# Performance work log

Hardware: AMD Instinct MI355X
Metric: run time of the kernel (lower is better)

Reference implementation:

```python
import jax, jax.numpy as jnp
import numpy as np

B, S, IN_F, OUT_F = 4, 2048, 4096, 4096
ALPHA = 0.01

def setup_inputs() -> dict:
    key = jax.random.key(0)
    k1, k2 = jax.random.split(key, 2)
    # int8-valued activations and weights (stored as int32 per harness dtype)
    x = jax.random.randint(k1, (B, S, IN_F), -127, 127, dtype=jnp.int32)
    weight = jax.random.randint(k2, (IN_F, OUT_F), -127, 127, dtype=jnp.int32)
    bias = jnp.zeros((1, OUT_F), dtype=jnp.float16)
    alpha = jnp.full((1,), ALPHA, dtype=jnp.float32)
    return {"x": x, "weight": weight, "bias": bias, "alpha": alpha}

def reference(x, weight, bias, alpha):
    # Faithful to forward's default (non-hybrid) path:
    # y = F.linear(x.float(), weight.t().float(), bias.float()) * alpha
    # F.linear(x, W^T) == x @ W, with W shape (in_features, out_features).
    x_shape = x.shape
    xf = x.reshape(-1, x_shape[-1]).astype(jnp.float32)          # [B*S, in]
    wf = weight.astype(jnp.float32)                               # [in, out]
    y = (xf @ wf + bias.astype(jnp.float32)) * alpha              # [B*S, out]
    return y.reshape(*x_shape[:-1], -1)                           # [B, S, out]
```

## Files before the change

kernel.cpp:

```cpp
#include <hip/hip_runtime.h>
#include <hip/hip_fp16.h>

using i32x4  = __attribute__((ext_vector_type(4)))  int;
using i32x16 = __attribute__((ext_vector_type(16))) int;

static constexpr int M  = 4 * 2048;
static constexpr int N  = 4096;
static constexpr int K  = 4096;
static constexpr int BM = 128, BN = 128, BK = 64;
static constexpr int NT = K / BK;
static constexpr int TILE = BM * BK;


__device__ __forceinline__ unsigned pack4(i32x4 v) {
  return (unsigned)((v.x & 255) | ((v.y & 255) << 8) | ((v.z & 255) << 16) | (v.w << 24));
}

__global__ __launch_bounds__(256) void pack_x_kernel(const int* __restrict__ x,
                                                     unsigned char* __restrict__ wa) {
  unsigned g = blockIdx.x * 256 + threadIdx.x;
  unsigned tile = g >> 9, gt = g & 511;
  unsigned kg = gt >> 7, row = gt & 127;
  unsigned br = tile >> 6, kt = tile & 63;
  const int* src = x + ((size_t)(br * 128 + row) * K + kt * 64 + kg * 16);
  i32x4 v0 = *(const i32x4*)(src + 0);
  i32x4 v1 = *(const i32x4*)(src + 4);
  i32x4 v2 = *(const i32x4*)(src + 8);
  i32x4 v3 = *(const i32x4*)(src + 12);
  i32x4 d;
  d.x = (int)pack4(v0); d.y = (int)pack4(v1); d.z = (int)pack4(v2); d.w = (int)pack4(v3);
  *(i32x4*)(wa + (size_t)g * 16) = d;
}

__global__ __launch_bounds__(256) void pack_w_kernel(const int* __restrict__ w,
                                                     unsigned char* __restrict__ wb) {
  unsigned g = blockIdx.x * 256 + threadIdx.x;
  unsigned tile = g >> 9, gt = g & 511;
  unsigned kg = gt >> 7, col = gt & 127;
  unsigned bn = tile >> 6, kt = tile & 63;
  unsigned n  = bn * 128 + col;
  unsigned k0 = kt * 64 + kg * 16;
  const int* src = w + (size_t)k0 * N + n;
  i32x4 d;
#pragma unroll
  for (int j = 0; j < 4; ++j) {
    int b0 = src[(size_t)(j * 4 + 0) * N];
    int b1 = src[(size_t)(j * 4 + 1) * N];
    int b2 = src[(size_t)(j * 4 + 2) * N];
    int b3 = src[(size_t)(j * 4 + 3) * N];
    d[j] = (b0 & 255) | ((b1 & 255) << 8) | ((b2 & 255) << 16) | (b3 << 24);
  }
  *(i32x4*)(wb + (size_t)g * 16) = d;
}


__device__ __forceinline__ void gload_lds16(const void* g, void* l) {
  __builtin_amdgcn_global_load_lds((const __attribute__((address_space(1))) unsigned int*)g,
                                   (__attribute__((address_space(3))) unsigned int*)l,
                                   16, 0, 0);
}

__global__ __launch_bounds__(256) void gemm_i8(const unsigned char* __restrict__ wa,
                                               const unsigned char* __restrict__ wb,
                                               const __half* __restrict__ bias,
                                               const float* __restrict__ alphaP,
                                               float* __restrict__ out) {
  __shared__ __align__(16) unsigned char As[2][TILE];
  __shared__ __align__(16) unsigned char Bs[2][TILE];

  const int tid  = threadIdx.x;
  const int lane = tid & 63;
  const int w    = tid >> 6;
  const int wr   = w >> 1, wc = w & 1;
  const int bc   = blockIdx.x, br = blockIdx.y;

  const unsigned char* ga = wa + (size_t)br * NT * TILE;
  const unsigned char* gb = wb + (size_t)bc * NT * TILE;

  i32x16 acc[2][2] = {};

  const int l31 = lane & 31;
  const int kgl = lane >> 5;

  auto stage = [&](int buf, int t) {
    const unsigned char* at = ga + (size_t)t * TILE;
    const unsigned char* bt = gb + (size_t)t * TILE;
#pragma unroll
    for (int i = 0; i < 2; ++i) {
      const int seg = w * 2 + i;
      gload_lds16(at + seg * 1024 + lane * 16, &As[buf][seg * 1024]);
      gload_lds16(bt + seg * 1024 + lane * 16, &Bs[buf][seg * 1024]);
    }
  };

  stage(0, 0);
  asm volatile("s_waitcnt vmcnt(0)" ::: "memory");
  __syncthreads();

  int cur = 0;
  for (int t = 0; t < NT; ++t) {
    if (t + 1 < NT) stage(cur ^ 1, t + 1);
#pragma unroll
    for (int c = 0; c < 2; ++c) {
      const int kg = c * 2 + kgl;
      const unsigned char* Ap = &As[cur][kg * 2048];
      const unsigned char* Bp = &Bs[cur][kg * 2048];
      i32x4 a0 = *(const i32x4*)(Ap + (wr * 64 + l31) * 16);
      i32x4 a1 = *(const i32x4*)(Ap + (wr * 64 + 32 + l31) * 16);
      i32x4 b0 = *(const i32x4*)(Bp + (wc * 64 + l31) * 16);
      i32x4 b1 = *(const i32x4*)(Bp + (wc * 64 + 32 + l31) * 16);
      acc[0][0] = __builtin_amdgcn_mfma_i32_32x32x32_i8(a0, b0, acc[0][0], 0, 0, 0);
      acc[0][1] = __builtin_amdgcn_mfma_i32_32x32x32_i8(a0, b1, acc[0][1], 0, 0, 0);
      acc[1][0] = __builtin_amdgcn_mfma_i32_32x32x32_i8(a1, b0, acc[1][0], 0, 0, 0);
      acc[1][1] = __builtin_amdgcn_mfma_i32_32x32x32_i8(a1, b1, acc[1][1], 0, 0, 0);
    }
    asm volatile("s_waitcnt vmcnt(0)" ::: "memory");
    __syncthreads();
    cur ^= 1;
  }

  const float alpha = *alphaP;
  const int row0 = br * 128 + wr * 64 + 4 * kgl;
  const int col0 = bc * 128 + wc * 64 + l31;
#pragma unroll
  for (int ni = 0; ni < 2; ++ni) {
    const int col = col0 + ni * 32;
    const float bf = __half2float(bias[col]);
#pragma unroll
    for (int mi = 0; mi < 2; ++mi) {
#pragma unroll
      for (int r = 0; r < 16; ++r) {
        const int row = row0 + mi * 32 + (r & 3) + 8 * (r >> 2);
        out[(size_t)row * N + col] = ((float)acc[mi][ni][r] + bf) * alpha;
      }
    }
  }
}

extern "C" void kernel_launch(void* const* d_in, const int* in_sizes, int n_in,
                              void* d_out, int out_size, void* d_ws, size_t ws_size,
                              hipStream_t stream) {
  const int*    x     = (const int*)d_in[0];
  const int*    wgt   = (const int*)d_in[1];
  const __half* bias  = (const __half*)d_in[2];
  const float*  alpha = (const float*)d_in[3];
  float*        out   = (float*)d_out;

  unsigned char* wa = (unsigned char*)d_ws;
  unsigned char* wb = wa + (size_t)M * K;

  pack_x_kernel<<<(M * (size_t)K / 16) / 256, 256, 0, stream>>>(x, wa);
  pack_w_kernel<<<(N * (size_t)K / 16) / 256, 256, 0, stream>>>(wgt, wb);

  dim3 grid(N / BN, M / BM);
  gemm_i8<<<grid, 256, 0, stream>>>(wa, wb, bias, alpha, out);
}
```

Measured before the change: 232.8 us.

## Enlarge GEMM tiles to 256x256 with 3-stage LDS pipeline and block swizzle

Doubles the block tile to 256x256 with 512 threads (8 waves, each 128x64), raising arithmetic intensity per LDS/global byte. Replaces the double buffer with a three-buffer prefetch pipeline using partial vmcnt waits, preloads fragments to registers before issuing the next stage, and raises MFMA priority. Adds a grid swizzle for L2 locality and repacks the pack kernels to the new tile layout. Risks higher register pressure (128 accumulator VGPRs per lane) and 96KB LDS limiting occupancy.

```diff
diff --git a/kernel.cpp b/kernel.cpp
--- a/kernel.cpp
+++ b/kernel.cpp
@@ -7,7 +7,7 @@
 static constexpr int M  = 4 * 2048;
 static constexpr int N  = 4096;
 static constexpr int K  = 4096;
-static constexpr int BM = 128, BN = 128, BK = 64;
+static constexpr int BM = 256, BN = 256, BK = 64;
 static constexpr int NT = K / BK;
 static constexpr int TILE = BM * BK;
 
@@ -19,10 +19,11 @@
 __global__ __launch_bounds__(256) void pack_x_kernel(const int* __restrict__ x,
                                                      unsigned char* __restrict__ wa) {
   unsigned g = blockIdx.x * 256 + threadIdx.x;
-  unsigned tile = g >> 9, gt = g & 511;
-  unsigned kg = gt >> 7, row = gt & 127;
-  unsigned br = tile >> 6, kt = tile & 63;
-  const int* src = x + ((size_t)(br * 128 + row) * K + kt * 64 + kg * 16);
+  unsigned row = g & 255;
+  unsigned kg  = (g >> 8) & 3;
+  unsigned kt  = (g >> 10) & 63;
+  unsigned br  = g >> 16;
+  const int* src = x + ((size_t)(br * 256 + row) * K + kt * 64 + kg * 16);
   i32x4 v0 = *(const i32x4*)(src + 0);
   i32x4 v1 = *(const i32x4*)(src + 4);
   i32x4 v2 = *(const i32x4*)(src + 8);
@@ -35,11 +36,12 @@
 __global__ __launch_bounds__(256) void pack_w_kernel(const int* __restrict__ w,
                                                      unsigned char* __restrict__ wb) {
   unsigned g = blockIdx.x * 256 + threadIdx.x;
-  unsigned tile = g >> 9, gt = g & 511;
-  unsigned kg = gt >> 7, col = gt & 127;
-  unsigned bn = tile >> 6, kt = tile & 63;
-  unsigned n  = bn * 128 + col;
-  unsigned k0 = kt * 64 + kg * 16;
+  unsigned col = g & 255;
+  unsigned kg  = (g >> 8) & 3;
+  unsigned kt  = (g >> 10) & 63;
+  unsigned bn  = g >> 16;
+  unsigned n   = bn * 256 + col;
+  unsigned k0  = kt * 64 + kg * 16;
   const int* src = w + (size_t)k0 * N + n;
   i32x4 d;
 #pragma unroll
@@ -60,74 +62,94 @@
                                    16, 0, 0);
 }
 
-__global__ __launch_bounds__(256) void gemm_i8(const unsigned char* __restrict__ wa,
-                                               const unsigned char* __restrict__ wb,
-                                               const __half* __restrict__ bias,
-                                               const float* __restrict__ alphaP,
-                                               float* __restrict__ out) {
-  __shared__ __align__(16) unsigned char As[2][TILE];
-  __shared__ __align__(16) unsigned char Bs[2][TILE];
+#define FENCE()   asm volatile("" ::: "memory")
+#define BARRIER() do { FENCE(); __builtin_amdgcn_s_barrier(); FENCE(); } while (0)
+
+__global__ __launch_bounds__(512, 2) void gemm_i8(const unsigned char* __restrict__ wa,
+                                                  const unsigned char* __restrict__ wb,
+                                                  const __half* __restrict__ bias,
+                                                  const float* __restrict__ alphaP,
+                                                  float* __restrict__ out) {
+  __shared__ __align__(16) unsigned char As[3][TILE];
+  __shared__ __align__(16) unsigned char Bs[3][TILE];
 
   const int tid  = threadIdx.x;
   const int lane = tid & 63;
   const int w    = tid >> 6;
-  const int wr   = w >> 1, wc = w & 1;
-  const int bc   = blockIdx.x, br = blockIdx.y;
+  const int wr   = w >> 2, wc = w & 3;
+  const int l31  = lane & 31;
+  const int kgl  = lane >> 5;
+
+  const int bid = blockIdx.x;
+  const int swz = (bid & 7) * 64 + (bid >> 3);
+  const int bc  = swz & 15;
+  const int br  = swz >> 4;
 
   const unsigned char* ga = wa + (size_t)br * NT * TILE;
   const unsigned char* gb = wb + (size_t)bc * NT * TILE;
 
-  i32x16 acc[2][2] = {};
-
-  const int l31 = lane & 31;
-  const int kgl = lane >> 5;
-
   auto stage = [&](int buf, int t) {
     const unsigned char* at = ga + (size_t)t * TILE;
     const unsigned char* bt = gb + (size_t)t * TILE;
-#pragma unroll
-    for (int i = 0; i < 2; ++i) {
-      const int seg = w * 2 + i;
-      gload_lds16(at + seg * 1024 + lane * 16, &As[buf][seg * 1024]);
-      gload_lds16(bt + seg * 1024 + lane * 16, &Bs[buf][seg * 1024]);
-    }
+    gload_lds16(at + w * 1024 + lane * 16,        &As[buf][w * 1024]);
+    gload_lds16(at + 8192 + w * 1024 + lane * 16, &As[buf][8192 + w * 1024]);
+    gload_lds16(bt + w * 1024 + lane * 16,        &Bs[buf][w * 1024]);
+    gload_lds16(bt + 8192 + w * 1024 + lane * 16, &Bs[buf][8192 + w * 1024]);
   };
 
   stage(0, 0);
-  asm volatile("s_waitcnt vmcnt(0)" ::: "memory");
-  __syncthreads();
+  stage(1, 1);
+  stage(2, 2);
 
-  int cur = 0;
+  i32x16 acc[4][2] = {};
+
+  int buf = 0;
   for (int t = 0; t < NT; ++t) {
-    if (t + 1 < NT) stage(cur ^ 1, t + 1);
+    if (t + 2 < NT)      asm volatile("s_waitcnt vmcnt(8)" ::: "memory");
+    else if (t + 1 < NT) asm volatile("s_waitcnt vmcnt(4)" ::: "memory");
+    else                 asm volatile("s_waitcnt vmcnt(0)" ::: "memory");
+    BARRIER();
+
+    i32x4 a[2][4], b[2][2];
 #pragma unroll
-    for (int c = 0; c < 2; ++c) {
-      const int kg = c * 2 + kgl;
-      const unsigned char* Ap = &As[cur][kg * 2048];
-      const unsigned char* Bp = &Bs[cur][kg * 2048];
-      i32x4 a0 = *(const i32x4*)(Ap + (wr * 64 + l31) * 16);
-      i32x4 a1 = *(const i32x4*)(Ap + (wr * 64 + 32 + l31) * 16);
-      i32x4 b0 = *(const i32x4*)(Bp + (wc * 64 + l31) * 16);
-      i32x4 b1 = *(const i32x4*)(Bp + (wc * 64 + 32 + l31) * 16);
-      acc[0][0] = __builtin_amdgcn_mfma_i32_32x32x32_i8(a0, b0, acc[0][0], 0, 0, 0);
-      acc[0][1] = __builtin_amdgcn_mfma_i32_32x32x32_i8(a0, b1, acc[0][1], 0, 0, 0);
-      acc[1][0] = __builtin_amdgcn_mfma_i32_32x32x32_i8(a1, b0, acc[1][0], 0, 0, 0);
-      acc[1][1] = __builtin_amdgcn_mfma_i32_32x32x32_i8(a1, b1, acc[1][1], 0, 0, 0);
+    for (int kc = 0; kc < 2; ++kc) {
+      const int kg = kc * 2 + kgl;
+      const unsigned char* Ap = &As[buf][kg * 4096];
+      const unsigned char* Bp = &Bs[buf][kg * 4096];
+#pragma unroll
+      for (int mi = 0; mi < 4; ++mi)
+        a[kc][mi] = *(const i32x4*)(Ap + (wr * 128 + mi * 32 + l31) * 16);
+#pragma unroll
+      for (int ni = 0; ni < 2; ++ni)
+        b[kc][ni] = *(const i32x4*)(Bp + (wc * 64 + ni * 32 + l31) * 16);
     }
-    asm volatile("s_waitcnt vmcnt(0)" ::: "memory");
-    __syncthreads();
-    cur ^= 1;
+    asm volatile("s_waitcnt lgkmcnt(0)" ::: "memory");
+    BARRIER();
+    if (t + 3 < NT) stage(buf, t + 3);
+
+    __builtin_amdgcn_s_setprio(1);
+#pragma unroll
+    for (int kc = 0; kc < 2; ++kc)
+#pragma unroll
+      for (int mi = 0; mi < 4; ++mi)
+#pragma unroll
+        for (int ni = 0; ni < 2; ++ni)
+          acc[mi][ni] = __builtin_amdgcn_mfma_i32_32x32x32_i8(a[kc][mi], b[kc][ni],
+                                                              acc[mi][ni], 0, 0, 0);
+    __builtin_amdgcn_s_setprio(0);
+
+    buf = (buf == 2) ? 0 : buf + 1;
   }
 
   const float alpha = *alphaP;
-  const int row0 = br * 128 + wr * 64 + 4 * kgl;
-  const int col0 = bc * 128 + wc * 64 + l31;
+  const int row0 = br * 256 + wr * 128 + 4 * kgl;
+  const int col0 = bc * 256 + wc * 64 + l31;
 #pragma unroll
   for (int ni = 0; ni < 2; ++ni) {
     const int col = col0 + ni * 32;
     const float bf = __half2float(bias[col]);
 #pragma unroll
-    for (int mi = 0; mi < 2; ++mi) {
+    for (int mi = 0; mi < 4; ++mi) {
 #pragma unroll
       for (int r = 0; r < 16; ++r) {
         const int row = row0 + mi * 32 + (r & 3) + 8 * (r >> 2);
@@ -152,6 +174,6 @@
   pack_x_kernel<<<(M * (size_t)K / 16) / 256, 256, 0, stream>>>(x, wa);
   pack_w_kernel<<<(N * (size_t)K / 16) / 256, 256, 0, stream>>>(wgt, wb);
 
-  dim3 grid(N / BN, M / BM);
-  gemm_i8<<<grid, 256, 0, stream>>>(wa, wb, bias, alpha, out);
+  dim3 grid((M / BM) * (N / BN));
+  gemm_i8<<<grid, 512, 0, stream>>>(wa, wb, bias, alpha, out);
 }
```

New measurement: 231.3 us. Within noise of the previous version (-0.6%).

## Enlarge GEMM M-tile to 256 and use triple-buffered LDS pipeline

Applied to the files above, without the earlier changes.

Doubles the block M-tile to 256 rows so each wave computes a 128x64 output using eight MFMA accumulators, which raises arithmetic intensity per LDS byte. The LDS pipeline moves from double to triple buffering with prefetch two tiles ahead and a partial vmcnt wait. The pack kernels are re-laid out to match the new tile geometry. In exchange it uses more registers and LDS per block, which may limit occupancy, and it adds pipeline complexity.

```diff
diff --git a/kernel.cpp b/kernel.cpp
--- a/kernel.cpp
+++ b/kernel.cpp
@@ -7,9 +7,10 @@
 static constexpr int M  = 4 * 2048;
 static constexpr int N  = 4096;
 static constexpr int K  = 4096;
-static constexpr int BM = 128, BN = 128, BK = 64;
+static constexpr int BM = 256, BN = 128, BK = 64;
 static constexpr int NT = K / BK;
-static constexpr int TILE = BM * BK;
+static constexpr int ATILE = BM * BK;
+static constexpr int BTILE = BN * BK;
 
 
 __device__ __forceinline__ unsigned pack4(i32x4 v) {
@@ -19,10 +20,11 @@
 __global__ __launch_bounds__(256) void pack_x_kernel(const int* __restrict__ x,
                                                      unsigned char* __restrict__ wa) {
   unsigned g = blockIdx.x * 256 + threadIdx.x;
-  unsigned tile = g >> 9, gt = g & 511;
-  unsigned kg = gt >> 7, row = gt & 127;
-  unsigned br = tile >> 6, kt = tile & 63;
-  const int* src = x + ((size_t)(br * 128 + row) * K + kt * 64 + kg * 16);
+  unsigned row = g & 255;
+  unsigned kg  = (g >> 8) & 3;
+  unsigned kt  = (g >> 10) & 63;
+  unsigned br  = g >> 16;
+  const int* src = x + ((size_t)(br * 256 + row) * K + kt * 64 + kg * 16);
   i32x4 v0 = *(const i32x4*)(src + 0);
   i32x4 v1 = *(const i32x4*)(src + 4);
   i32x4 v2 = *(const i32x4*)(src + 8);
@@ -35,11 +37,12 @@
 __global__ __launch_bounds__(256) void pack_w_kernel(const int* __restrict__ w,
                                                      unsigned char* __restrict__ wb) {
   unsigned g = blockIdx.x * 256 + threadIdx.x;
-  unsigned tile = g >> 9, gt = g & 511;
-  unsigned kg = gt >> 7, col = gt & 127;
-  unsigned bn = tile >> 6, kt = tile & 63;
-  unsigned n  = bn * 128 + col;
-  unsigned k0 = kt * 64 + kg * 16;
+  unsigned col = g & 127;
+  unsigned kg  = (g >> 7) & 3;
+  unsigned kt  = (g >> 9) & 63;
+  unsigned bn  = g >> 15;
+  unsigned n   = bn * 128 + col;
+  unsigned k0  = kt * 64 + kg * 16;
   const int* src = w + (size_t)k0 * N + n;
   i32x4 d;
 #pragma unroll
@@ -60,74 +63,88 @@
                                    16, 0, 0);
 }
 
-__global__ __launch_bounds__(256) void gemm_i8(const unsigned char* __restrict__ wa,
-                                               const unsigned char* __restrict__ wb,
-                                               const __half* __restrict__ bias,
-                                               const float* __restrict__ alphaP,
-                                               float* __restrict__ out) {
-  __shared__ __align__(16) unsigned char As[2][TILE];
-  __shared__ __align__(16) unsigned char Bs[2][TILE];
+__global__ __launch_bounds__(256, 2) void gemm_i8(const unsigned char* __restrict__ wa,
+                                                  const unsigned char* __restrict__ wb,
+                                                  const __half* __restrict__ bias,
+                                                  const float* __restrict__ alphaP,
+                                                  float* __restrict__ out) {
+  __shared__ __align__(16) unsigned char As[3][ATILE];
+  __shared__ __align__(16) unsigned char Bs[3][BTILE];
 
   const int tid  = threadIdx.x;
   const int lane = tid & 63;
   const int w    = tid >> 6;
   const int wr   = w >> 1, wc = w & 1;
-  const int bc   = blockIdx.x, br = blockIdx.y;
+  const int l31  = lane & 31;
+  const int kgl  = lane >> 5;
 
-  const unsigned char* ga = wa + (size_t)br * NT * TILE;
-  const unsigned char* gb = wb + (size_t)bc * NT * TILE;
+  const int bc = blockIdx.x;
+  const int br = blockIdx.y;
 
-  i32x16 acc[2][2] = {};
-
-  const int l31 = lane & 31;
-  const int kgl = lane >> 5;
+  const unsigned char* ga = wa + (size_t)br * NT * ATILE;
+  const unsigned char* gb = wb + (size_t)bc * NT * BTILE;
 
   auto stage = [&](int buf, int t) {
-    const unsigned char* at = ga + (size_t)t * TILE;
-    const unsigned char* bt = gb + (size_t)t * TILE;
+    const unsigned char* at = ga + (size_t)t * ATILE;
+    const unsigned char* bt = gb + (size_t)t * BTILE;
 #pragma unroll
-    for (int i = 0; i < 2; ++i) {
-      const int seg = w * 2 + i;
-      gload_lds16(at + seg * 1024 + lane * 16, &As[buf][seg * 1024]);
-      gload_lds16(bt + seg * 1024 + lane * 16, &Bs[buf][seg * 1024]);
-    }
+    for (int j = 0; j < 4; ++j)
+      gload_lds16(at + (w * 4 + j) * 1024 + lane * 16, &As[buf][(w * 4 + j) * 1024]);
+#pragma unroll
+    for (int j = 0; j < 2; ++j)
+      gload_lds16(bt + (w * 2 + j) * 1024 + lane * 16, &Bs[buf][(w * 2 + j) * 1024]);
   };
 
   stage(0, 0);
-  asm volatile("s_waitcnt vmcnt(0)" ::: "memory");
-  __syncthreads();
+  stage(1, 1);
+  asm volatile("s_waitcnt vmcnt(6)" ::: "memory");
+  __builtin_amdgcn_s_barrier();
 
-  int cur = 0;
+  i32x16 acc[4][2] = {};
+
+  const int arow = wr * 128 + l31;
+  const int bcol = wc * 64 + l31;
+
   for (int t = 0; t < NT; ++t) {
-    if (t + 1 < NT) stage(cur ^ 1, t + 1);
+    if (t + 2 < NT) stage((t + 2) % 3, t + 2);
+
+    const unsigned char* Ab = &As[t % 3][0] + kgl * 4096;
+    const unsigned char* Bb = &Bs[t % 3][0] + kgl * 2048;
+
 #pragma unroll
-    for (int c = 0; c < 2; ++c) {
-      const int kg = c * 2 + kgl;
-      const unsigned char* Ap = &As[cur][kg * 2048];
-      const unsigned char* Bp = &Bs[cur][kg * 2048];
-      i32x4 a0 = *(const i32x4*)(Ap + (wr * 64 + l31) * 16);
-      i32x4 a1 = *(const i32x4*)(Ap + (wr * 64 + 32 + l31) * 16);
-      i32x4 b0 = *(const i32x4*)(Bp + (wc * 64 + l31) * 16);
-      i32x4 b1 = *(const i32x4*)(Bp + (wc * 64 + 32 + l31) * 16);
+    for (int kc = 0; kc < 2; ++kc) {
+      const unsigned char* Ap = Ab + kc * 8192;
+      const unsigned char* Bp = Bb + kc * 4096;
+      i32x4 a0 = *(const i32x4*)(Ap + (arow +  0) * 16);
+      i32x4 a1 = *(const i32x4*)(Ap + (arow + 32) * 16);
+      i32x4 a2 = *(const i32x4*)(Ap + (arow + 64) * 16);
+      i32x4 a3 = *(const i32x4*)(Ap + (arow + 96) * 16);
+      i32x4 b0 = *(const i32x4*)(Bp + (bcol +  0) * 16);
+      i32x4 b1 = *(const i32x4*)(Bp + (bcol + 32) * 16);
       acc[0][0] = __builtin_amdgcn_mfma_i32_32x32x32_i8(a0, b0, acc[0][0], 0, 0, 0);
       acc[0][1] = __builtin_amdgcn_mfma_i32_32x32x32_i8(a0, b1, acc[0][1], 0, 0, 0);
       acc[1][0] = __builtin_amdgcn_mfma_i32_32x32x32_i8(a1, b0, acc[1][0], 0, 0, 0);
       acc[1][1] = __builtin_amdgcn_mfma_i32_32x32x32_i8(a1, b1, acc[1][1], 0, 0, 0);
+      acc[2][0] = __builtin_amdgcn_mfma_i32_32x32x32_i8(a2, b0, acc[2][0], 0, 0, 0);
+      acc[2][1] = __builtin_amdgcn_mfma_i32_32x32x32_i8(a2, b1, acc[2][1], 0, 0, 0);
+      acc[3][0] = __builtin_amdgcn_mfma_i32_32x32x32_i8(a3, b0, acc[3][0], 0, 0, 0);
+      acc[3][1] = __builtin_amdgcn_mfma_i32_32x32x32_i8(a3, b1, acc[3][1], 0, 0, 0);
     }
-    asm volatile("s_waitcnt vmcnt(0)" ::: "memory");
-    __syncthreads();
-    cur ^= 1;
+
+    if (t + 2 < NT)      asm volatile("s_waitcnt vmcnt(6)" ::: "memory");
+    else if (t + 1 < NT) asm volatile("s_waitcnt vmcnt(0)" ::: "memory");
+    __builtin_amdgcn_s_barrier();
   }
 
   const float alpha = *alphaP;
-  const int row0 = br * 128 + wr * 64 + 4 * kgl;
+  const int row0 = br * 256 + wr * 128 + 4 * kgl;
   const int col0 = bc * 128 + wc * 64 + l31;
 #pragma unroll
   for (int ni = 0; ni < 2; ++ni) {
     const int col = col0 + ni * 32;
     const float bf = __half2float(bias[col]);
 #pragma unroll
-    for (int mi = 0; mi < 2; ++mi) {
+    for (int mi = 0; mi < 4; ++mi) {
 #pragma unroll
       for (int r = 0; r < 16; ++r) {
         const int row = row0 + mi * 32 + (r & 3) + 8 * (r >> 2);
```

Measured after the change: 242.4 us. +4.1%, slower.
